# Optimization experiments

Measured on AMD Instinct MI355X. Metric: run time of the kernel, lower is better.

Reference implementation:

```python
import jax, jax.numpy as jnp
import numpy as np

B, L, H, DK, DV, DM = 8, 1024, 8, 80, 80, 640
LN_EPS = 1e-5


def setup_inputs() -> dict:
    key = jax.random.key(0)
    ks = jax.random.split(key, 5)
    q = jax.random.normal(ks[0], (B, L, DM), dtype=jnp.float32)
    k = jax.random.normal(ks[1], (B, L, DM), dtype=jnp.float32)
    v = jax.random.normal(ks[2], (B, L, DM), dtype=jnp.float32)
    # fc: nn.Linear(n_head*d_v, d_model), xavier-normal init
    fc_std = float(np.sqrt(2.0 / (H * DV + DM)))
    fc_w = jax.random.normal(ks[3], (DM, H * DV), dtype=jnp.float32) * fc_std
    fc_b = jnp.zeros((DM,), dtype=jnp.float32)
    gamma_1 = jnp.full((DM,), 1e-4, dtype=jnp.float32)  # init_values * ones(640)
    ln_w = jnp.ones((DM,), dtype=jnp.float32)
    ln_b = jnp.zeros((DM,), dtype=jnp.float32)
    return {"q": q, "k": k, "v": v, "fc_w": fc_w, "fc_b": fc_b,
            "gamma_1": gamma_1, "ln_w": ln_w, "ln_b": ln_b}


def reference(q, k, v, fc_w, fc_b, gamma_1, ln_w, ln_b):
    # Inputs are viewed directly into heads (projections are commented out in source).
    residual = q
    qh = q.reshape(B, L, H, DK)  # [b, q, h, d]
    kh = k.reshape(B, L, H, DK)  # [b, k, h, d]
    vh = v.reshape(B, L, H, DV)  # [b, k, h, d]

    # L2-distance attention scores: -sum((q-k)^2) = -(||q||^2 - 2 q.k + ||k||^2)
    sq = jnp.sum(qh * qh, axis=-1)                       # [b, q, h]
    sk = jnp.sum(kh * kh, axis=-1)                       # [b, k, h]
    cross = jnp.einsum('bqhd,bkhd->bhqk', qh, kh)        # [b, h, q, k]
    scores = -(sq.transpose(0, 2, 1)[:, :, :, None]
               - 2.0 * cross
               + sk.transpose(0, 2, 1)[:, :, None, :]) / 13.0

    attn = jax.nn.softmax(scores, axis=-1)               # softmax over keys (dim=2 in 3D view)
    # dropout(p=0.8) treated as identity (eval mode)

    out = jnp.einsum('bhqk,bkhd->bqhd', attn, vh)        # [b, q, h, dv]
    out = out.reshape(B, L, H * DV)
    out = out @ fc_w.T + fc_b                            # fc projection
    # dropout treated as identity (eval mode)

    x = out * gamma_1 + residual
    mu = jnp.mean(x, axis=-1, keepdims=True)
    var = jnp.mean((x - mu) ** 2, axis=-1, keepdims=True)
    y = (x - mu) * jax.lax.rsqrt(var + LN_EPS) * ln_w + ln_b
    return y
```

## Files before the change

kernel.cpp:

```cpp
#include <hip/hip_runtime.h>

#define B_ 8
#define L_ 1024
#define H_ 8
#define DM_ 640

typedef __attribute__((ext_vector_type(8))) short bf16x8;
typedef __attribute__((ext_vector_type(4))) short bf16x4;
typedef __attribute__((ext_vector_type(4))) float f32x4;
typedef __attribute__((ext_vector_type(2))) float f32x2;
typedef __attribute__((ext_vector_type(4))) int i32x4;
typedef __attribute__((ext_vector_type(2))) int i32x2;
typedef __attribute__((ext_vector_type(4))) unsigned short us4;
typedef __attribute__((ext_vector_type(8))) unsigned short us8;

#if __has_builtin(__builtin_amdgcn_exp2f)
#define EXP2F __builtin_amdgcn_exp2f
#else
#define EXP2F exp2f
#endif

#define C1F 0.22195308f
#define C2F 0.11097654f

#define VTP_TILE_SHORTS 5184
#define ATTN8_OFF 10616832

__device__ __forceinline__ unsigned short f2bf(float f) {
  unsigned int u = __builtin_bit_cast(unsigned int, f);
  u += 0x7fffu + ((u >> 16) & 1u);
  return (unsigned short)(u >> 16);
}
__device__ __forceinline__ float bf2f(unsigned short h) {
  unsigned int u = ((unsigned int)h) << 16;
  return __builtin_bit_cast(float, u);
}
__device__ __forceinline__ float sane(float x, float lim) {
  return fminf(fmaxf(x, -lim), lim);
}
__device__ __forceinline__ unsigned cvt_pk_bf16(float a, float b) {
  unsigned r;
  asm("v_cvt_pk_bf16_f32 %0, %1, %2" : "=v"(r) : "v"(a), "v"(b));
  return r;
}

__global__ __launch_bounds__(256) void prep_kernel(
    const float* __restrict__ kg, const float* __restrict__ vg,
    unsigned short* __restrict__ Kp, unsigned short* __restrict__ Vtp) {
  __shared__ float V_lds[64 * 81];
  __shared__ float w_lds[64];
  const int tid = threadIdx.x;
  const int bh = blockIdx.x >> 4, kt = blockIdx.x & 15;
  const int b = bh >> 3, h = bh & 7;
  const int key = tid >> 2, part = tid & 3;
  const int keyg = kt * 64 + key;

  const float* krow = kg + (size_t)(b * L_ + keyg) * DM_ + h * 80 + part * 20;
  const float* vrow = vg + (size_t)(b * L_ + keyg) * DM_ + h * 80 + part * 20;
  unsigned short* kpr = Kp + ((size_t)bh * L_ + keyg) * 80 + part * 20;

  float ssq = 0.f;
#pragma unroll
  for (int i = 0; i < 5; ++i) {
    float4 f = *(const float4*)(krow + 4 * i);
    ssq += f.x * f.x + f.y * f.y + f.z * f.z + f.w * f.w;
    us4 h4 = {f2bf(f.x * C1F), f2bf(f.y * C1F), f2bf(f.z * C1F), f2bf(f.w * C1F)};
    *(us4*)(kpr + 4 * i) = h4;
    float4 g4 = *(const float4*)(vrow + 4 * i);
    int d0 = part * 20 + 4 * i;
    V_lds[key * 81 + d0 + 0] = g4.x;
    V_lds[key * 81 + d0 + 1] = g4.y;
    V_lds[key * 81 + d0 + 2] = g4.z;
    V_lds[key * 81 + d0 + 3] = g4.w;
  }
  ssq += __shfl_xor(ssq, 1);
  ssq += __shfl_xor(ssq, 2);
  if (part == 0) w_lds[key] = EXP2F((80.f - ssq) * C2F);
  __syncthreads();

  unsigned short* vt = Vtp + (size_t)(bh * 16 + kt) * VTP_TILE_SHORTS;
#pragma unroll
  for (int r = 0; r < 11; ++r) {
    int p = r * 256 + tid;
    if (p < 81 * 32) {
      int dv = p >> 5, kp = (p & 31) * 2;
      float wa = w_lds[kp], wb = w_lds[kp + 1];
      float va = (dv < 80) ? V_lds[kp * 81 + dv] * wa : wa;
      float vb = (dv < 80) ? V_lds[(kp + 1) * 81 + dv] * wb : wb;
      *(unsigned*)(vt + dv * 64 + kp) =
          (unsigned)f2bf(va) | ((unsigned)f2bf(vb) << 16);
    }
  }
}

#define KSTR 104
#define VSTR 76

__global__ __launch_bounds__(256, 2) void attn_kernel(
    const float* __restrict__ qg, const unsigned short* __restrict__ Kp,
    const unsigned short* __restrict__ Vtp, unsigned char* __restrict__ attn8) {
  __shared__ __align__(16) unsigned short K_lds[2][64 * KSTR];
  __shared__ __align__(16) unsigned short Vt_lds[2][96 * VSTR];

  const int tid = threadIdx.x;
  const int wid = tid >> 6, lane = tid & 63;
  const int col = lane & 15, g = lane >> 4;
  const int bx = blockIdx.x;
  const int bh = bx & 63, qt = bx >> 6;
  const int b = bh >> 3, h = bh & 7;

  {
    us8 z = {0, 0, 0, 0, 0, 0, 0, 0};
    if (tid < 128) {
      int bufz = tid >> 6, r = tid & 63;
      *(us8*)&K_lds[bufz][r * KSTR + 80] = z;
      *(us8*)&K_lds[bufz][r * KSTR + 88] = z;
    }
    if (tid < 240) {
      int bufz = tid / 120, t2 = tid % 120;
      int vr = 81 + (t2 >> 3), hc = t2 & 7;
      *(us8*)&Vt_lds[bufz][vr * VSTR + hc * 8] = z;
    }
  }

  const int ka0 = tid, ka1 = tid + 256, ka2 = tid + 512;
  const int kr0 = ka0 / 10, kc0 = ka0 - kr0 * 10;
  const int kr1 = ka1 / 10, kc1 = ka1 - kr1 * 10;
  const int kr2 = ka2 / 10, kc2 = ka2 - kr2 * 10;
  const int vr0 = ka0 >> 3, vc0 = ka0 & 7;
  const int vr1 = ka1 >> 3, vc1 = ka1 & 7;
  const int vr2 = ka2 >> 3, vc2 = ka2 & 7;

  const unsigned short* kslice = Kp + (size_t)bh * L_ * 80;
  const unsigned short* vslice = Vtp + (size_t)(bh * 16) * VTP_TILE_SHORTS;

  us8 sk0, sk1, sk2, sv0, sv1, sv2;
  auto load_tile = [&](int kt) {
    const unsigned short* kb = kslice + (size_t)kt * 5120;
    const unsigned short* vb = vslice + (size_t)kt * VTP_TILE_SHORTS;
    sk0 = *(const us8*)(kb + kr0 * 80 + kc0 * 8);
    sk1 = *(const us8*)(kb + kr1 * 80 + kc1 * 8);
    if (tid < 128) sk2 = *(const us8*)(kb + kr2 * 80 + kc2 * 8);
    sv0 = *(const us8*)(vb + vr0 * 64 + vc0 * 8);
    sv1 = *(const us8*)(vb + vr1 * 64 + vc1 * 8);
    if (tid < 136) sv2 = *(const us8*)(vb + vr2 * 64 + vc2 * 8);
  };
  auto write_tile = [&](int bf) {
    *(us8*)&K_lds[bf][kr0 * KSTR + kc0 * 8] = sk0;
    *(us8*)&K_lds[bf][kr1 * KSTR + kc1 * 8] = sk1;
    if (tid < 128) *(us8*)&K_lds[bf][kr2 * KSTR + kc2 * 8] = sk2;
    *(us8*)&Vt_lds[bf][vr0 * VSTR + vc0 * 8] = sv0;
    *(us8*)&Vt_lds[bf][vr1 * VSTR + vc1 * 8] = sv1;
    if (tid < 136) *(us8*)&Vt_lds[bf][vr2 * VSTR + vc2 * 8] = sv2;
  };

  bf16x8 qa0[3], qa1[3];
  {
    const int qr0 = qt * 128 + wid * 16 + col;
#pragma unroll
    for (int s = 0; s < 2; ++s) {
      const float* qr = qg + (size_t)(b * L_ + qr0 + s * 64) * DM_ + h * 80;
      bf16x8* qa = s ? qa1 : qa0;
#pragma unroll
      for (int c = 0; c < 3; ++c) {
        int d0 = c * 32 + g * 8;
        if (d0 < 80) {
          float4 f0 = *(const float4*)(qr + d0);
          float4 f1 = *(const float4*)(qr + d0 + 4);
          qa[c][0] = (short)f2bf(f0.x); qa[c][1] = (short)f2bf(f0.y);
          qa[c][2] = (short)f2bf(f0.z); qa[c][3] = (short)f2bf(f0.w);
          qa[c][4] = (short)f2bf(f1.x); qa[c][5] = (short)f2bf(f1.y);
          qa[c][6] = (short)f2bf(f1.z); qa[c][7] = (short)f2bf(f1.w);
        } else {
#pragma unroll
          for (int e = 0; e < 8; ++e) qa[c][e] = 0;
        }
      }
    }
  }

  f32x4 acc_o0[6], acc_o1[6];
#pragma unroll
  for (int u = 0; u < 6; ++u) {
    f32x4 z = {0.f, 0.f, 0.f, 0.f};
    acc_o0[u] = z;
    acc_o1[u] = z;
  }

  load_tile(0);
  write_tile(0);
  __syncthreads();

  for (int kt = 0; kt < 16; ++kt) {
    const int cur = kt & 1;
    if (kt < 15) load_tile(kt + 1);

    f32x4 accS0[4], accS1[4];
#pragma unroll
    for (int t = 0; t < 4; ++t) {
      f32x4 z = {0.f, 0.f, 0.f, 0.f};
      accS0[t] = z;
      accS1[t] = z;
    }
#pragma unroll
    for (int t = 0; t < 4; ++t)
#pragma unroll
      for (int c = 0; c < 3; ++c) {
        bf16x8 kf =
            *(const bf16x8*)&K_lds[cur][(t * 16 + col) * KSTR + c * 32 + g * 8];
        accS0[t] = __builtin_amdgcn_mfma_f32_16x16x32_bf16(kf, qa0[c], accS0[t], 0, 0, 0);
        accS1[t] = __builtin_amdgcn_mfma_f32_16x16x32_bf16(kf, qa1[c], accS1[t], 0, 0, 0);
      }

    unsigned pkA0[4], pkB0[4], pkA1[4], pkB1[4];
#pragma unroll
    for (int t = 0; t < 4; ++t) {
      pkA0[t] = cvt_pk_bf16(EXP2F(accS0[t][0]), EXP2F(accS0[t][1]));
      pkB0[t] = cvt_pk_bf16(EXP2F(accS0[t][2]), EXP2F(accS0[t][3]));
      pkA1[t] = cvt_pk_bf16(EXP2F(accS1[t][0]), EXP2F(accS1[t][1]));
      pkB1[t] = cvt_pk_bf16(EXP2F(accS1[t][2]), EXP2F(accS1[t][3]));
    }

#if __has_builtin(__builtin_amdgcn_mfma_f32_16x16x16bf16_1k)
#pragma unroll
    for (int t = 0; t < 4; ++t) {
      i32x2 pw0 = {(int)pkA0[t], (int)pkB0[t]};
      i32x2 pw1 = {(int)pkA1[t], (int)pkB1[t]};
      bf16x4 pf0 = __builtin_bit_cast(bf16x4, pw0);
      bf16x4 pf1 = __builtin_bit_cast(bf16x4, pw1);
#pragma unroll
      for (int u = 0; u < 6; ++u) {
        bf16x4 vf =
            *(const bf16x4*)&Vt_lds[cur][(u * 16 + col) * VSTR + t * 16 + g * 4];
        acc_o0[u] = __builtin_amdgcn_mfma_f32_16x16x16bf16_1k(vf, pf0, acc_o0[u], 0, 0, 0);
        acc_o1[u] = __builtin_amdgcn_mfma_f32_16x16x16bf16_1k(vf, pf1, acc_o1[u], 0, 0, 0);
      }
    }
#else
    const int g1 = g & 1, g2 = g >> 1;
#pragma unroll
    for (int s = 0; s < 2; ++s) {
      unsigned* pkA = s ? pkA1 : pkA0;
      unsigned* pkB = s ? pkB1 : pkB0;
      f32x4* acc_o = s ? acc_o1 : acc_o0;
#pragma unroll
      for (int c = 0; c < 2; ++c) {
        int A0 = pkA[2 * c], A1 = pkA[2 * c + 1];
        int B0 = pkB[2 * c], B1 = pkB[2 * c + 1];
        int a16 = __shfl_xor(A0, 16), a32 = __shfl_xor(A0, 32), a48 = __shfl_xor(A0, 48);
        int c16 = __shfl_xor(A1, 16), c32 = __shfl_xor(A1, 32), c48 = __shfl_xor(A1, 48);
        int b16 = __shfl_xor(B0, 16), b32 = __shfl_xor(B0, 32), b48 = __shfl_xor(B0, 48);
        int d16 = __shfl_xor(B1, 16), d32 = __shfl_xor(B1, 32), d48 = __shfl_xor(B1, 48);
        int W0 = g2 ? (g1 ? c16 : c32) : (g1 ? a48 : A0);
        int W1 = g2 ? (g1 ? d16 : d32) : (g1 ? b48 : B0);
        int W2 = g2 ? (g1 ? A1 : c48) : (g1 ? a32 : a16);
        int W3 = g2 ? (g1 ? B1 : d48) : (g1 ? b32 : b16);
        i32x4 wv = {W0, W1, W2, W3};
        bf16x8 pf = __builtin_bit_cast(bf16x8, wv);
#pragma unroll
        for (int u = 0; u < 6; ++u) {
          bf16x8 vf =
              *(const bf16x8*)&Vt_lds[cur][(u * 16 + col) * VSTR + c * 32 + g * 8];
          acc_o[u] = __builtin_amdgcn_mfma_f32_16x16x32_bf16(vf, pf, acc_o[u], 0, 0, 0);
        }
      }
    }
#endif

    if (kt < 15) {
      write_tile(cur ^ 1);
      __syncthreads();
    }
  }

#pragma unroll
  for (int s = 0; s < 2; ++s) {
    f32x4* acc_o = s ? acc_o1 : acc_o0;
    float l = __shfl(acc_o[5][0], col);
    float invl = 1.0f / fmaxf(l, 1e-30f);
    const int qrow = qt * 128 + s * 64 + wid * 16 + col;
    unsigned char* ob = attn8 + (size_t)(b * L_ + qrow) * DM_ + h * 80;
#pragma unroll
    for (int u = 0; u < 5; ++u) {
      float o0 = sane(acc_o[u][0] * invl, 240.f);
      float o1 = sane(acc_o[u][1] * invl, 240.f);
      float o2 = sane(acc_o[u][2] * invl, 240.f);
      float o3 = sane(acc_o[u][3] * invl, 240.f);
      int pk = __builtin_amdgcn_cvt_pk_fp8_f32(o0, o1, 0, false);
      pk = __builtin_amdgcn_cvt_pk_fp8_f32(o2, o3, pk, true);
      *(int*)(ob + u * 16 + g * 4) = pk;
    }
  }
}

#define BSTR 40
__global__ __launch_bounds__(256) void fc_kernel(
    const unsigned char* __restrict__ attn8, const float* __restrict__ w,
    const float* __restrict__ fcb, const float* __restrict__ gamma,
    const float* __restrict__ qres, unsigned short* __restrict__ xout) {
  __shared__ __align__(16) unsigned short A_lds[2][128 * BSTR];
  __shared__ __align__(16) unsigned short B_lds[2][128 * BSTR];

  const int tid = threadIdx.x;
  const int wid = tid >> 6, lane = tid & 63;
  const int col = lane & 15, g = lane >> 4;
  const int rt = blockIdx.x / 5, ct = blockIdx.x % 5;
  const int wm = wid >> 1, wn = wid & 1;
  const int r = tid >> 1, seg = tid & 1;

  f32x4 acc[4][4];
#pragma unroll
  for (int m = 0; m < 4; ++m)
#pragma unroll
    for (int n = 0; n < 4; ++n) {
      f32x4 z = {0.f, 0.f, 0.f, 0.f};
      acc[m][n] = z;
    }

  uint4 sa;
  float4 sb[4];
  auto load_k = [&](int kc) {
    sa = *(const uint4*)(attn8 + (size_t)(rt * 128 + r) * DM_ + kc * 32 + seg * 16);
    const float* wsrc = w + (size_t)(ct * 128 + r) * DM_ + kc * 32 + seg * 16;
#pragma unroll
    for (int i = 0; i < 4; ++i) sb[i] = *(const float4*)(wsrc + 4 * i);
  };
  auto write_k = [&](int bf) {
    const unsigned* adw = (const unsigned*)&sa;
#pragma unroll
    for (int wde = 0; wde < 4; ++wde) {
      f32x2 lo = __builtin_amdgcn_cvt_pk_f32_fp8(adw[wde], false);
      f32x2 hi = __builtin_amdgcn_cvt_pk_f32_fp8(adw[wde], true);
      us4 h4 = {f2bf(lo[0]), f2bf(lo[1]), f2bf(hi[0]), f2bf(hi[1])};
      *(us4*)&A_lds[bf][r * BSTR + seg * 16 + wde * 4] = h4;
    }
#pragma unroll
    for (int i = 0; i < 4; ++i) {
      us4 h4 = {f2bf(sb[i].x), f2bf(sb[i].y), f2bf(sb[i].z), f2bf(sb[i].w)};
      *(us4*)&B_lds[bf][r * BSTR + seg * 16 + 4 * i] = h4;
    }
  };

  load_k(0);
  write_k(0);
  __syncthreads();

  for (int kc = 0; kc < 20; ++kc) {
    const int cur = kc & 1;
    if (kc < 19) load_k(kc + 1);

    bf16x8 af[4], bfr[4];
#pragma unroll
    for (int m = 0; m < 4; ++m)
      af[m] = *(const bf16x8*)&A_lds[cur][(wm * 64 + m * 16 + col) * BSTR + g * 8];
#pragma unroll
    for (int n = 0; n < 4; ++n)
      bfr[n] = *(const bf16x8*)&B_lds[cur][(wn * 64 + n * 16 + col) * BSTR + g * 8];
#pragma unroll
    for (int m = 0; m < 4; ++m)
#pragma unroll
      for (int n = 0; n < 4; ++n)
        acc[m][n] = __builtin_amdgcn_mfma_f32_16x16x32_bf16(af[m], bfr[n], acc[m][n], 0, 0, 0);

    if (kc < 19) {
      write_k(cur ^ 1);
      __syncthreads();
    }
  }

  int jcol[4];
  float fb4[4], gm[4];
#pragma unroll
  for (int n = 0; n < 4; ++n) {
    jcol[n] = ct * 128 + wn * 64 + n * 16 + col;
    fb4[n] = fcb[jcol[n]];
    gm[n] = gamma[jcol[n]];
  }
#pragma unroll
  for (int m = 0; m < 4; ++m) {
    int rowg = rt * 128 + wm * 64 + m * 16 + g * 4;
#pragma unroll
    for (int j = 0; j < 4; ++j) {
      int row = rowg + j;
#pragma unroll
      for (int n = 0; n < 4; ++n) {
        float xv = (acc[m][n][j] + fb4[n]) * gm[n] + qres[(size_t)row * DM_ + jcol[n]];
        xout[(size_t)row * DM_ + jcol[n]] = f2bf(sane(xv, 1e5f));
      }
    }
  }
}

__global__ __launch_bounds__(256) void ln_kernel(
    const unsigned short* __restrict__ x, const float* __restrict__ lw,
    const float* __restrict__ lb, float* __restrict__ y) {
  const int wid = threadIdx.x >> 6, lane = threadIdx.x & 63;
  const int row = blockIdx.x * 4 + wid;
  const unsigned short* xr = x + (size_t)row * DM_;

  unsigned int u[5];
  float s = 0.f, ss = 0.f;
#pragma unroll
  for (int i = 0; i < 5; ++i) {
    u[i] = *(const unsigned int*)(xr + 2 * (lane + 64 * i));
    float a0 = bf2f((unsigned short)(u[i] & 0xffff));
    float a1 = bf2f((unsigned short)(u[i] >> 16));
    s += a0 + a1;
    ss += a0 * a0 + a1 * a1;
  }
#pragma unroll
  for (int d = 1; d < 64; d <<= 1) {
    s += __shfl_xor(s, d);
    ss += __shfl_xor(ss, d);
  }
  const float mu = s * (1.f / 640.f);
  const float var = ss * (1.f / 640.f) - mu * mu;
  const float rstd = rsqrtf(var + 1e-5f);

  float* yr = y + (size_t)row * DM_;
#pragma unroll
  for (int i = 0; i < 5; ++i) {
    int c0 = 2 * (lane + 64 * i);
    float a0 = bf2f((unsigned short)(u[i] & 0xffff));
    float a1 = bf2f((unsigned short)(u[i] >> 16));
    float2 wv = *(const float2*)(lw + c0);
    float2 bv = *(const float2*)(lb + c0);
    float2 out;
    out.x = (a0 - mu) * rstd * wv.x + bv.x;
    out.y = (a1 - mu) * rstd * wv.y + bv.y;
    *(float2*)(yr + c0) = out;
  }
}

extern "C" void kernel_launch(void* const* d_in, const int* in_sizes, int n_in,
                              void* d_out, int out_size, void* d_ws, size_t ws_size,
                              hipStream_t stream) {
  const float* q = (const float*)d_in[0];
  const float* k = (const float*)d_in[1];
  const float* v = (const float*)d_in[2];
  const float* fw = (const float*)d_in[3];
  const float* fb = (const float*)d_in[4];
  const float* g1 = (const float*)d_in[5];
  const float* lw = (const float*)d_in[6];
  const float* lb = (const float*)d_in[7];

  unsigned short* vtp = (unsigned short*)d_out;
  unsigned char* attn8 = (unsigned char*)d_out + ATTN8_OFF;
  unsigned short* kp = (unsigned short*)d_ws;
  unsigned short* xws = (unsigned short*)d_ws;
  float* y = (float*)d_out;

  prep_kernel<<<dim3(64 * 16), dim3(256), 0, stream>>>(k, v, kp, vtp);
  attn_kernel<<<dim3(64 * 8), dim3(256), 0, stream>>>(q, kp, vtp, attn8);
  fc_kernel<<<dim3((8192 / 128) * 5), dim3(256), 0, stream>>>(attn8, fw, fb, g1, q, xws);
  ln_kernel<<<dim3(8192 / 4), dim3(256), 0, stream>>>(xws, lw, lb, y);
}
```

Before: 86.09 us.

## Halve attention block size, single-buffer LDS, compute softmax denominator from weights

The attention kernel now runs 128-thread blocks covering 64 query rows instead of 256 threads covering 128, which doubles the grid to 1024 blocks. K/V staging drops from double-buffered LDS to a single buffer guarded by two barriers per tile. The softmax denominator is no longer taken from an extra ones-column MFMA output (the 6th V tile). It is now accumulated in registers from exp values times per-key weights read from a small shared array, then reduced across lanes. This removes one sixth of the PV MFMAs and cuts LDS use, which may raise occupancy, but adds barrier stalls and less latency hiding.

```diff
diff --git a/kernel.cpp b/kernel.cpp
--- a/kernel.cpp
+++ b/kernel.cpp
@@ -9,8 +9,8 @@
 typedef __attribute__((ext_vector_type(4))) short bf16x4;
 typedef __attribute__((ext_vector_type(4))) float f32x4;
 typedef __attribute__((ext_vector_type(2))) float f32x2;
+typedef __attribute__((ext_vector_type(2))) int i32x2;
 typedef __attribute__((ext_vector_type(4))) int i32x4;
-typedef __attribute__((ext_vector_type(2))) int i32x2;
 typedef __attribute__((ext_vector_type(4))) unsigned short us4;
 typedef __attribute__((ext_vector_type(8))) unsigned short us8;
 
@@ -96,11 +96,12 @@
 #define KSTR 104
 #define VSTR 76
 
-__global__ __launch_bounds__(256, 2) void attn_kernel(
+__global__ __launch_bounds__(128) void attn_kernel(
     const float* __restrict__ qg, const unsigned short* __restrict__ Kp,
     const unsigned short* __restrict__ Vtp, unsigned char* __restrict__ attn8) {
-  __shared__ __align__(16) unsigned short K_lds[2][64 * KSTR];
-  __shared__ __align__(16) unsigned short Vt_lds[2][96 * VSTR];
+  __shared__ __align__(16) unsigned short K_lds[64 * KSTR];
+  __shared__ __align__(16) unsigned short Vt_lds[80 * VSTR];
+  __shared__ __align__(16) unsigned short w_sh[64];
 
   const int tid = threadIdx.x;
   const int wid = tid >> 6, lane = tid & 63;
@@ -109,57 +110,50 @@
   const int bh = bx & 63, qt = bx >> 6;
   const int b = bh >> 3, h = bh & 7;
 
-  {
+  if (tid < 64) {
     us8 z = {0, 0, 0, 0, 0, 0, 0, 0};
-    if (tid < 128) {
-      int bufz = tid >> 6, r = tid & 63;
-      *(us8*)&K_lds[bufz][r * KSTR + 80] = z;
-      *(us8*)&K_lds[bufz][r * KSTR + 88] = z;
-    }
-    if (tid < 240) {
-      int bufz = tid / 120, t2 = tid % 120;
-      int vr = 81 + (t2 >> 3), hc = t2 & 7;
-      *(us8*)&Vt_lds[bufz][vr * VSTR + hc * 8] = z;
-    }
-  }
-
-  const int ka0 = tid, ka1 = tid + 256, ka2 = tid + 512;
-  const int kr0 = ka0 / 10, kc0 = ka0 - kr0 * 10;
-  const int kr1 = ka1 / 10, kc1 = ka1 - kr1 * 10;
-  const int kr2 = ka2 / 10, kc2 = ka2 - kr2 * 10;
-  const int vr0 = ka0 >> 3, vc0 = ka0 & 7;
-  const int vr1 = ka1 >> 3, vc1 = ka1 & 7;
-  const int vr2 = ka2 >> 3, vc2 = ka2 & 7;
-
+    *(us8*)&K_lds[tid * KSTR + 80] = z;
+    *(us8*)&K_lds[tid * KSTR + 88] = z;
+  }
+
+  int krr[5], kcc[5], vrr[5], vcc[5];
+#pragma unroll
+  for (int i = 0; i < 5; ++i) {
+    int f = tid + 128 * i;
+    krr[i] = f / 10;
+    kcc[i] = f - krr[i] * 10;
+    vrr[i] = f >> 3;
+    vcc[i] = f & 7;
+  }
   const unsigned short* kslice = Kp + (size_t)bh * L_ * 80;
   const unsigned short* vslice = Vtp + (size_t)(bh * 16) * VTP_TILE_SHORTS;
 
-  us8 sk0, sk1, sk2, sv0, sv1, sv2;
+  us8 sk[5], sv[5], sw;
   auto load_tile = [&](int kt) {
     const unsigned short* kb = kslice + (size_t)kt * 5120;
     const unsigned short* vb = vslice + (size_t)kt * VTP_TILE_SHORTS;
-    sk0 = *(const us8*)(kb + kr0 * 80 + kc0 * 8);
-    sk1 = *(const us8*)(kb + kr1 * 80 + kc1 * 8);
-    if (tid < 128) sk2 = *(const us8*)(kb + kr2 * 80 + kc2 * 8);
-    sv0 = *(const us8*)(vb + vr0 * 64 + vc0 * 8);
-    sv1 = *(const us8*)(vb + vr1 * 64 + vc1 * 8);
-    if (tid < 136) sv2 = *(const us8*)(vb + vr2 * 64 + vc2 * 8);
+#pragma unroll
+    for (int i = 0; i < 5; ++i) {
+      sk[i] = *(const us8*)(kb + krr[i] * 80 + kcc[i] * 8);
+      sv[i] = *(const us8*)(vb + vrr[i] * 64 + vcc[i] * 8);
+    }
+    if (tid < 8) sw = *(const us8*)(vb + 5120 + tid * 8);
   };
-  auto write_tile = [&](int bf) {
-    *(us8*)&K_lds[bf][kr0 * KSTR + kc0 * 8] = sk0;
-    *(us8*)&K_lds[bf][kr1 * KSTR + kc1 * 8] = sk1;
-    if (tid < 128) *(us8*)&K_lds[bf][kr2 * KSTR + kc2 * 8] = sk2;
-    *(us8*)&Vt_lds[bf][vr0 * VSTR + vc0 * 8] = sv0;
-    *(us8*)&Vt_lds[bf][vr1 * VSTR + vc1 * 8] = sv1;
-    if (tid < 136) *(us8*)&Vt_lds[bf][vr2 * VSTR + vc2 * 8] = sv2;
+  auto write_tile = [&]() {
+#pragma unroll
+    for (int i = 0; i < 5; ++i) {
+      *(us8*)&K_lds[krr[i] * KSTR + kcc[i] * 8] = sk[i];
+      *(us8*)&Vt_lds[vrr[i] * VSTR + vcc[i] * 8] = sv[i];
+    }
+    if (tid < 8) *(us8*)&w_sh[tid * 8] = sw;
   };
 
   bf16x8 qa0[3], qa1[3];
   {
-    const int qr0 = qt * 128 + wid * 16 + col;
+    const int qr0 = qt * 64 + wid * 16 + col;
 #pragma unroll
     for (int s = 0; s < 2; ++s) {
-      const float* qr = qg + (size_t)(b * L_ + qr0 + s * 64) * DM_ + h * 80;
+      const float* qr = qg + (size_t)(b * L_ + qr0 + s * 32) * DM_ + h * 80;
       bf16x8* qa = s ? qa1 : qa0;
 #pragma unroll
       for (int c = 0; c < 3; ++c) {
@@ -179,20 +173,21 @@
     }
   }
 
-  f32x4 acc_o0[6], acc_o1[6];
-#pragma unroll
-  for (int u = 0; u < 6; ++u) {
+  f32x4 acc_o0[5], acc_o1[5];
+#pragma unroll
+  for (int u = 0; u < 5; ++u) {
     f32x4 z = {0.f, 0.f, 0.f, 0.f};
     acc_o0[u] = z;
     acc_o1[u] = z;
   }
+  float lp0 = 0.f, lp1 = 0.f;
 
   load_tile(0);
-  write_tile(0);
-  __syncthreads();
 
   for (int kt = 0; kt < 16; ++kt) {
-    const int cur = kt & 1;
+    __syncthreads();
+    write_tile();
+    __syncthreads();
     if (kt < 15) load_tile(kt + 1);
 
     f32x4 accS0[4], accS1[4];
@@ -206,79 +201,43 @@
     for (int t = 0; t < 4; ++t)
 #pragma unroll
       for (int c = 0; c < 3; ++c) {
-        bf16x8 kf =
-            *(const bf16x8*)&K_lds[cur][(t * 16 + col) * KSTR + c * 32 + g * 8];
+        bf16x8 kf = *(const bf16x8*)&K_lds[(t * 16 + col) * KSTR + c * 32 + g * 8];
         accS0[t] = __builtin_amdgcn_mfma_f32_16x16x32_bf16(kf, qa0[c], accS0[t], 0, 0, 0);
         accS1[t] = __builtin_amdgcn_mfma_f32_16x16x32_bf16(kf, qa1[c], accS1[t], 0, 0, 0);
       }
 
-    unsigned pkA0[4], pkB0[4], pkA1[4], pkB1[4];
 #pragma unroll
     for (int t = 0; t < 4; ++t) {
-      pkA0[t] = cvt_pk_bf16(EXP2F(accS0[t][0]), EXP2F(accS0[t][1]));
-      pkB0[t] = cvt_pk_bf16(EXP2F(accS0[t][2]), EXP2F(accS0[t][3]));
-      pkA1[t] = cvt_pk_bf16(EXP2F(accS1[t][0]), EXP2F(accS1[t][1]));
-      pkB1[t] = cvt_pk_bf16(EXP2F(accS1[t][2]), EXP2F(accS1[t][3]));
-    }
-
-#if __has_builtin(__builtin_amdgcn_mfma_f32_16x16x16bf16_1k)
-#pragma unroll
-    for (int t = 0; t < 4; ++t) {
-      i32x2 pw0 = {(int)pkA0[t], (int)pkB0[t]};
-      i32x2 pw1 = {(int)pkA1[t], (int)pkB1[t]};
+      us4 w4 = *(const us4*)&w_sh[t * 16 + g * 4];
+      float w0 = bf2f(w4[0]), w1 = bf2f(w4[1]), w2 = bf2f(w4[2]), w3 = bf2f(w4[3]);
+      float p00 = EXP2F(accS0[t][0]), p01 = EXP2F(accS0[t][1]);
+      float p02 = EXP2F(accS0[t][2]), p03 = EXP2F(accS0[t][3]);
+      float p10 = EXP2F(accS1[t][0]), p11 = EXP2F(accS1[t][1]);
+      float p12 = EXP2F(accS1[t][2]), p13 = EXP2F(accS1[t][3]);
+      lp0 += p00 * w0 + p01 * w1 + p02 * w2 + p03 * w3;
+      lp1 += p10 * w0 + p11 * w1 + p12 * w2 + p13 * w3;
+      i32x2 pw0 = {(int)cvt_pk_bf16(p00, p01), (int)cvt_pk_bf16(p02, p03)};
+      i32x2 pw1 = {(int)cvt_pk_bf16(p10, p11), (int)cvt_pk_bf16(p12, p13)};
       bf16x4 pf0 = __builtin_bit_cast(bf16x4, pw0);
       bf16x4 pf1 = __builtin_bit_cast(bf16x4, pw1);
 #pragma unroll
-      for (int u = 0; u < 6; ++u) {
-        bf16x4 vf =
-            *(const bf16x4*)&Vt_lds[cur][(u * 16 + col) * VSTR + t * 16 + g * 4];
+      for (int u = 0; u < 5; ++u) {
+        bf16x4 vf = *(const bf16x4*)&Vt_lds[(u * 16 + col) * VSTR + t * 16 + g * 4];
         acc_o0[u] = __builtin_amdgcn_mfma_f32_16x16x16bf16_1k(vf, pf0, acc_o0[u], 0, 0, 0);
         acc_o1[u] = __builtin_amdgcn_mfma_f32_16x16x16bf16_1k(vf, pf1, acc_o1[u], 0, 0, 0);
       }
     }
-#else
-    const int g1 = g & 1, g2 = g >> 1;
-#pragma unroll
-    for (int s = 0; s < 2; ++s) {
-      unsigned* pkA = s ? pkA1 : pkA0;
-      unsigned* pkB = s ? pkB1 : pkB0;
-      f32x4* acc_o = s ? acc_o1 : acc_o0;
-#pragma unroll
-      for (int c = 0; c < 2; ++c) {
-        int A0 = pkA[2 * c], A1 = pkA[2 * c + 1];
-        int B0 = pkB[2 * c], B1 = pkB[2 * c + 1];
-        int a16 = __shfl_xor(A0, 16), a32 = __shfl_xor(A0, 32), a48 = __shfl_xor(A0, 48);
-        int c16 = __shfl_xor(A1, 16), c32 = __shfl_xor(A1, 32), c48 = __shfl_xor(A1, 48);
-        int b16 = __shfl_xor(B0, 16), b32 = __shfl_xor(B0, 32), b48 = __shfl_xor(B0, 48);
-        int d16 = __shfl_xor(B1, 16), d32 = __shfl_xor(B1, 32), d48 = __shfl_xor(B1, 48);
-        int W0 = g2 ? (g1 ? c16 : c32) : (g1 ? a48 : A0);
-        int W1 = g2 ? (g1 ? d16 : d32) : (g1 ? b48 : B0);
-        int W2 = g2 ? (g1 ? A1 : c48) : (g1 ? a32 : a16);
-        int W3 = g2 ? (g1 ? B1 : d48) : (g1 ? b32 : b16);
-        i32x4 wv = {W0, W1, W2, W3};
-        bf16x8 pf = __builtin_bit_cast(bf16x8, wv);
-#pragma unroll
-        for (int u = 0; u < 6; ++u) {
-          bf16x8 vf =
-              *(const bf16x8*)&Vt_lds[cur][(u * 16 + col) * VSTR + c * 32 + g * 8];
-          acc_o[u] = __builtin_amdgcn_mfma_f32_16x16x32_bf16(vf, pf, acc_o[u], 0, 0, 0);
-        }
-      }
-    }
-#endif
-
-    if (kt < 15) {
-      write_tile(cur ^ 1);
-      __syncthreads();
-    }
-  }
-
+  }
+
+  float l0 = lp0 + __shfl_xor(lp0, 16);
+  l0 += __shfl_xor(l0, 32);
+  float l1 = lp1 + __shfl_xor(lp1, 16);
+  l1 += __shfl_xor(l1, 32);
 #pragma unroll
   for (int s = 0; s < 2; ++s) {
     f32x4* acc_o = s ? acc_o1 : acc_o0;
-    float l = __shfl(acc_o[5][0], col);
-    float invl = 1.0f / fmaxf(l, 1e-30f);
-    const int qrow = qt * 128 + s * 64 + wid * 16 + col;
+    float invl = 1.0f / fmaxf(s ? l1 : l0, 1e-30f);
+    const int qrow = qt * 64 + s * 32 + wid * 16 + col;
     unsigned char* ob = attn8 + (size_t)(b * L_ + qrow) * DM_ + h * 80;
 #pragma unroll
     for (int u = 0; u < 5; ++u) {
@@ -451,7 +410,7 @@
   float* y = (float*)d_out;
 
   prep_kernel<<<dim3(64 * 16), dim3(256), 0, stream>>>(k, v, kp, vtp);
-  attn_kernel<<<dim3(64 * 8), dim3(256), 0, stream>>>(q, kp, vtp, attn8);
+  attn_kernel<<<dim3(64 * 16), dim3(128), 0, stream>>>(q, kp, vtp, attn8);
   fc_kernel<<<dim3((8192 / 128) * 5), dim3(256), 0, stream>>>(attn8, fw, fb, g1, q, xws);
   ln_kernel<<<dim3(8192 / 4), dim3(256), 0, stream>>>(xws, lw, lb, y);
 }
```

After: 94.08 us. 9.3% more time.
